# Kernel optimization log

Measured on AMD Instinct MI355X. Metric: run time of the kernel, lower is better.

The kernel has to match this reference:

```python
import jax, jax.numpy as jnp
import numpy as np

B, Q, K, DQ, DK, H, DV = 4, 1024, 1024, 256, 256, 64, 256

def setup_inputs() -> dict:
    key = jax.random.key(0)
    k1, k2, k3, k4, k5, k6 = jax.random.split(key, 6)
    queries = jax.random.normal(k1, (B, Q, DQ), dtype=jnp.float32)
    keys = jax.random.normal(k2, (B, K, DK), dtype=jnp.float32)
    values = jax.random.normal(k3, (B, K, DV), dtype=jnp.float32)
    # learned params (stored as (in, out) so x @ W matches nn.Linear)
    W_q = jax.random.normal(k4, (DQ, H), dtype=jnp.float32) / np.sqrt(DQ)
    W_k = jax.random.normal(k5, (DK, H), dtype=jnp.float32) / np.sqrt(DK)
    w_v = jax.random.normal(k6, (H,), dtype=jnp.float32) / np.sqrt(H)
    return {"queries": queries, "keys": keys, "values": values,
            "W_q": W_q, "W_k": W_k, "w_v": w_v}

def reference(queries, keys, values, W_q, W_k, w_v):
    # projections: [B,Q,H], [B,K,H]
    q = jnp.einsum('bqd,dh->bqh', queries, W_q)
    k = jnp.einsum('bkd,dh->bkh', keys, W_k)
    # broadcast add -> tanh -> reduce with w_v: scores [B,Q,K]
    features = jnp.tanh(q[:, :, None, :] + k[:, None, :, :])  # [B,Q,K,H]
    scores = jnp.einsum('bqkh,h->bqk', features, w_v)
    attn = jax.nn.softmax(scores, axis=-1)  # dropout is identity in eval
    return jnp.einsum('bqk,bkv->bqv', attn, values)
```

## Files before the change

### kernel.cpp

```cpp
#include <hip/hip_runtime.h>

#define Bn 4
#define Qn 1024
#define Kn 1024
#define Dd 256
#define Hh 64
#define Dv 256
#define TQ 16

typedef __attribute__((ext_vector_type(8))) short short8;
typedef __attribute__((ext_vector_type(4))) float floatx4;
typedef __attribute__((ext_vector_type(2))) float floatx2;

__device__ __forceinline__ floatx2 fma2(floatx2 a, floatx2 b, floatx2 c) {
    return __builtin_elementwise_fma(a, b, c);
}
__device__ __forceinline__ floatx2 mk2(float x, float y) {
    floatx2 r; r.x = x; r.y = y; return r;
}

__device__ __forceinline__ short f32_to_bf16(float x) {
    unsigned u = __float_as_uint(x);
    unsigned r = u + 0x7fffu + ((u >> 16) & 1u);
    return (short)(r >> 16);
}
__device__ __forceinline__ float bf16_to_f32(short h) {
    return __uint_as_float(((unsigned)(unsigned short)h) << 16);
}

__global__ __launch_bounds__(256) void prep_kernel(const float* __restrict__ Xq,
                                                   const float* __restrict__ Wq,
                                                   const float* __restrict__ Xk,
                                                   const float* __restrict__ Wk,
                                                   const float* __restrict__ V,
                                                   float* __restrict__ Eq,
                                                   float* __restrict__ Ekt,
                                                   short* __restrict__ Vhi,
                                                   short* __restrict__ Vlo) {
    __shared__ float tile[32 * 261];
    int t = threadIdx.x;
    if (blockIdx.x < 256) {
        int gw = blockIdx.x * 4 + (t >> 6);
        int h = t & 63;
        int side = gw >> 9;
        int row0 = (gw & 511) * 8;
        const float* X = side ? Xk : Xq;
        const float* W = side ? Wk : Wq;
        float acc[8] = {0.f, 0.f, 0.f, 0.f, 0.f, 0.f, 0.f, 0.f};
        for (int d4 = 0; d4 < Dd / 4; ++d4) {
            float w0 = W[(d4 * 4 + 0) * Hh + h];
            float w1 = W[(d4 * 4 + 1) * Hh + h];
            float w2 = W[(d4 * 4 + 2) * Hh + h];
            float w3 = W[(d4 * 4 + 3) * Hh + h];
            #pragma unroll
            for (int r = 0; r < 8; ++r) {
                float4 xv = ((const float4*)(X + (size_t)(row0 + r) * Dd))[d4];
                acc[r] = fmaf(xv.x, w0, acc[r]);
                acc[r] = fmaf(xv.y, w1, acc[r]);
                acc[r] = fmaf(xv.z, w2, acc[r]);
                acc[r] = fmaf(xv.w, w3, acc[r]);
            }
        }
        #pragma unroll
        for (int r = 0; r < 8; ++r) {
            int row = row0 + r;
            float e = __expf(2.f * acc[r]);
            if (!side) {
                Eq[(size_t)row * Hh + h] = e;
            } else {
                int b = row >> 10, k = row & 1023;
                Ekt[((size_t)b * Hh + h) * Kn + k] = e;
            }
        }
    } else {
        int blk = blockIdx.x - 256;
        int b = blk >> 5;
        int kt = blk & 31;
        const float* Vg = V + (b * Kn + kt * 32) * Dv;
        for (int i = 0; i < 8; ++i) {
            int k = i * 4 + (t >> 6);
            int n4 = (t & 63) * 4;
            float4 v = *(const float4*)(Vg + k * Dv + n4);
            tile[k * 261 + n4 + 0] = v.x;
            tile[k * 261 + n4 + 1] = v.y;
            tile[k * 261 + n4 + 2] = v.z;
            tile[k * 261 + n4 + 3] = v.w;
        }
        __syncthreads();
        int wave = t >> 6, l = t & 63;
        int n_in = l & 15, kc = l >> 4;
        for (int p = 0; p < 4; ++p) {
            int nt = wave * 4 + p;
            int n = nt * 16 + n_in;
            short8 hi, lo;
            #pragma unroll
            for (int j = 0; j < 8; ++j) {
                float x = tile[(kc * 8 + j) * 261 + n];
                short hs = f32_to_bf16(x);
                hi[j] = hs;
                lo[j] = f32_to_bf16(x - bf16_to_f32(hs));
            }
            size_t base = (((size_t)(b * 32 + kt) * 16 + nt) * 512) + (size_t)l * 8;
            *(short8*)(Vhi + base) = hi;
            *(short8*)(Vlo + base) = lo;
        }
    }
}

__global__ __launch_bounds__(1024, 4) void attn_kernel(const float* __restrict__ Eq,
                                                       const float* __restrict__ Ekt,
                                                       const short* __restrict__ Vhi,
                                                       const short* __restrict__ Vlo,
                                                       const float* __restrict__ wv,
                                                       float* __restrict__ out) {
    __shared__ __align__(16) unsigned sc[TQ * 1028];
    __shared__ float wsum[16 * TQ];
    __shared__ float rinv_s[TQ];

    int tid = threadIdx.x;
    int blk = blockIdx.x;
    int b = (blk & 7) >> 1;
    int tile = (blk >> 3) * 2 + (blk & 1);
    int qbase = tile * TQ;

    const float* kb = Ekt + (size_t)b * Hh * Kn;
    const float* qp = Eq + (size_t)(b * Qn + qbase) * Hh;
    const float4* wv4 = (const float4*)wv;
    floatx2 s2[TQ / 2];
    #pragma unroll
    for (int i = 0; i < TQ / 2; ++i) { s2[i].x = 0.f; s2[i].y = 0.f; }

    float e0 = kb[0 * Kn + tid];
    float e1 = kb[1 * Kn + tid];
    float e2 = kb[2 * Kn + tid];
    float e3 = kb[3 * Kn + tid];
    floatx2 one2 = mk2(1.f, 1.f);
    for (int h4 = 0; h4 < Hh / 4; ++h4) {
        float n0, n1, n2, n3;
        if (h4 < Hh / 4 - 1) {
            const float* kn = kb + (h4 + 1) * 4 * Kn;
            n0 = kn[0 * Kn + tid];
            n1 = kn[1 * Kn + tid];
            n2 = kn[2 * Kn + tid];
            n3 = kn[3 * Kn + tid];
        }
        float4 w4 = wv4[h4];
        floatx2 e0s = mk2(e0, e0), e1s = mk2(e1, e1);
        floatx2 e2s = mk2(e2, e2), e3s = mk2(e3, e3);
        floatx2 wx = mk2(w4.x, w4.x), wy = mk2(w4.y, w4.y);
        floatx2 wz = mk2(w4.z, w4.z), ww = mk2(w4.w, w4.w);
        #pragma unroll
        for (int qq = 0; qq < TQ; qq += 2) {
            float4 qva = *(const float4*)(qp + qq * Hh + h4 * 4);
            float4 qvb = *(const float4*)(qp + (qq + 1) * Hh + h4 * 4);
            floatx2 A = fma2(mk2(qva.x, qvb.x), e0s, one2);
            floatx2 B = fma2(mk2(qva.y, qvb.y), e1s, one2);
            floatx2 C = fma2(mk2(qva.z, qvb.z), e2s, one2);
            floatx2 D = fma2(mk2(qva.w, qvb.w), e3s, one2);
            floatx2 AB = A * B;
            floatx2 CD = C * D;
            floatx2 ABCD = AB * CD;
            floatx2 NAB = fma2(wx, B, wy * A);
            floatx2 NCD = fma2(wz, D, ww * C);
            floatx2 NUM = fma2(NCD, AB, NAB * CD);
            floatx2 R = mk2(__builtin_amdgcn_rcpf(ABCD.x),
                            __builtin_amdgcn_rcpf(ABCD.y));
            s2[qq >> 1] = fma2(NUM, R, s2[qq >> 1]);
        }
        e0 = n0; e1 = n1; e2 = n2; e3 = n3;
    }

    unsigned short* sp = (unsigned short*)sc;
    float part[TQ];
    #pragma unroll
    for (int q = 0; q < TQ; ++q) {
        float sq = (q & 1) ? s2[q >> 1].y : s2[q >> 1].x;
        float p = __expf(-2.f * sq);
        part[q] = p;
        short hs = f32_to_bf16(p);
        sp[q * 2056 + tid] = (unsigned short)hs;
        sp[q * 2056 + 1024 + tid] = (unsigned short)f32_to_bf16(p - bf16_to_f32(hs));
    }

    int wave = tid >> 6, lane = tid & 63;
    #pragma unroll
    for (int q = 0; q < TQ; ++q) {
        #pragma unroll
        for (int off = 32; off >= 1; off >>= 1)
            part[q] += __shfl_xor(part[q], off, 64);
    }
    if (lane == 0) {
        #pragma unroll
        for (int q = 0; q < TQ; ++q) wsum[wave * TQ + q] = part[q];
    }
    __syncthreads();

    {
        float v = (lane < 16) ? wsum[lane * TQ + wave] : 0.f;
        v += __shfl_xor(v, 8, 64);
        v += __shfl_xor(v, 4, 64);
        v += __shfl_xor(v, 2, 64);
        v += __shfl_xor(v, 1, 64);
        if (lane == 0) rinv_s[wave] = 1.f / v;
    }
    __syncthreads();

    int qf = lane & 15, kc = lane >> 4;
    floatx4 acc = {0.f, 0.f, 0.f, 0.f};
    const char* scb = (const char*)sc;
    for (int kt = 0; kt < 32; ++kt) {
        short8 bhi = *(const short8*)(scb + qf * 4112 + kt * 64 + kc * 16);
        short8 blo = *(const short8*)(scb + qf * 4112 + 2048 + kt * 64 + kc * 16);
        size_t base = (((size_t)(b * 32 + kt) * 16 + wave) * 512) + (size_t)lane * 8;
        short8 ah = *(const short8*)(Vhi + base);
        short8 al = *(const short8*)(Vlo + base);
        acc = __builtin_amdgcn_mfma_f32_16x16x32_bf16(ah, bhi, acc, 0, 0, 0);
        acc = __builtin_amdgcn_mfma_f32_16x16x32_bf16(al, bhi, acc, 0, 0, 0);
        acc = __builtin_amdgcn_mfma_f32_16x16x32_bf16(ah, blo, acc, 0, 0, 0);
    }
    {
        float r = rinv_s[qf];
        float* ob = out + ((size_t)(b * Qn + qbase + qf)) * Dv + wave * 16 + kc * 4;
        float4 o = { acc[0] * r, acc[1] * r, acc[2] * r, acc[3] * r };
        *(float4*)ob = o;
    }
}

extern "C" void kernel_launch(void* const* d_in, const int* in_sizes, int n_in,
                              void* d_out, int out_size, void* d_ws, size_t ws_size,
                              hipStream_t stream) {
    const float* queries = (const float*)d_in[0];
    const float* keys    = (const float*)d_in[1];
    const float* values  = (const float*)d_in[2];
    const float* W_q     = (const float*)d_in[3];
    const float* W_k     = (const float*)d_in[4];
    const float* w_v     = (const float*)d_in[5];
    float* out = (float*)d_out;

    float* Eq  = (float*)d_ws;
    float* Ekt = Eq + Bn * Qn * Hh;
    short* Vhi = (short*)(Ekt + Bn * Kn * Hh);
    short* Vlo = Vhi + (size_t)Bn * Kn * Dv;

    prep_kernel<<<384, 256, 0, stream>>>(queries, W_q, keys, W_k, values,
                                         Eq, Ekt, Vhi, Vlo);
    attn_kernel<<<Bn * (Qn / TQ), 1024, 0, stream>>>(Eq, Ekt, Vhi, Vlo, w_v, out);
}
```

Measured before the change: 124.4 us.

## Split key dimension across two blocks with separate normalization kernel

Each attention block now handles half of the keys (512 threads instead of 1024), writing unnormalized partial outputs and partial softmax sums to workspace. A new norm kernel adds the two halves and divides by the combined sum. The aim is smaller blocks and twice as many of them for better occupancy and load balance. The cost is an extra kernel launch and extra global traffic for the partial results. Softmax has no max subtraction, so adding the partials is exact.

```diff
diff --git a/kernel.cpp b/kernel.cpp
--- a/kernel.cpp
+++ b/kernel.cpp
@@ -107,21 +107,23 @@
     }
 }
 
-__global__ __launch_bounds__(1024, 4) void attn_kernel(const float* __restrict__ Eq,
-                                                       const float* __restrict__ Ekt,
-                                                       const short* __restrict__ Vhi,
-                                                       const short* __restrict__ Vlo,
-                                                       const float* __restrict__ wv,
-                                                       float* __restrict__ out) {
-    __shared__ __align__(16) unsigned sc[TQ * 1028];
-    __shared__ float wsum[16 * TQ];
-    __shared__ float rinv_s[TQ];
+__global__ __launch_bounds__(512, 4) void attn_kernel(const float* __restrict__ Eq,
+                                                      const float* __restrict__ Ekt,
+                                                      const short* __restrict__ Vhi,
+                                                      const short* __restrict__ Vlo,
+                                                      const float* __restrict__ wv,
+                                                      float* __restrict__ Ows,
+                                                      float* __restrict__ Sws) {
+    __shared__ __align__(16) unsigned sc[TQ * 514];
+    __shared__ float wsum[8 * TQ];
 
     int tid = threadIdx.x;
     int blk = blockIdx.x;
     int b = (blk & 7) >> 1;
-    int tile = (blk >> 3) * 2 + (blk & 1);
+    int idx = (blk >> 3) * 2 + (blk & 1);
+    int tile = idx >> 1, half = idx & 1;
     int qbase = tile * TQ;
+    int kglob = half * 512 + tid;
 
     const float* kb = Ekt + (size_t)b * Hh * Kn;
     const float* qp = Eq + (size_t)(b * Qn + qbase) * Hh;
@@ -130,19 +132,19 @@
     #pragma unroll
     for (int i = 0; i < TQ / 2; ++i) { s2[i].x = 0.f; s2[i].y = 0.f; }
 
-    float e0 = kb[0 * Kn + tid];
-    float e1 = kb[1 * Kn + tid];
-    float e2 = kb[2 * Kn + tid];
-    float e3 = kb[3 * Kn + tid];
+    float e0 = kb[0 * Kn + kglob];
+    float e1 = kb[1 * Kn + kglob];
+    float e2 = kb[2 * Kn + kglob];
+    float e3 = kb[3 * Kn + kglob];
     floatx2 one2 = mk2(1.f, 1.f);
     for (int h4 = 0; h4 < Hh / 4; ++h4) {
         float n0, n1, n2, n3;
         if (h4 < Hh / 4 - 1) {
             const float* kn = kb + (h4 + 1) * 4 * Kn;
-            n0 = kn[0 * Kn + tid];
-            n1 = kn[1 * Kn + tid];
-            n2 = kn[2 * Kn + tid];
-            n3 = kn[3 * Kn + tid];
+            n0 = kn[0 * Kn + kglob];
+            n1 = kn[1 * Kn + kglob];
+            n2 = kn[2 * Kn + kglob];
+            n3 = kn[3 * Kn + kglob];
         }
         float4 w4 = wv4[h4];
         floatx2 e0s = mk2(e0, e0), e1s = mk2(e1, e1);
@@ -178,8 +180,8 @@
         float p = __expf(-2.f * sq);
         part[q] = p;
         short hs = f32_to_bf16(p);
-        sp[q * 2056 + tid] = (unsigned short)hs;
-        sp[q * 2056 + 1024 + tid] = (unsigned short)f32_to_bf16(p - bf16_to_f32(hs));
+        sp[q * 1028 + tid] = (unsigned short)hs;
+        sp[q * 1028 + 512 + tid] = (unsigned short)f32_to_bf16(p - bf16_to_f32(hs));
     }
 
     int wave = tid >> 6, lane = tid & 63;
@@ -195,34 +197,59 @@
     }
     __syncthreads();
 
-    {
-        float v = (lane < 16) ? wsum[lane * TQ + wave] : 0.f;
-        v += __shfl_xor(v, 8, 64);
+    #pragma unroll
+    for (int rr = 0; rr < 2; ++rr) {
+        int q = wave + rr * 8;
+        float v = (lane < 8) ? wsum[lane * TQ + q] : 0.f;
         v += __shfl_xor(v, 4, 64);
         v += __shfl_xor(v, 2, 64);
         v += __shfl_xor(v, 1, 64);
-        if (lane == 0) rinv_s[wave] = 1.f / v;
-    }
-    __syncthreads();
+        if (lane == 0)
+            Sws[(size_t)half * (Bn * Qn) + (size_t)(b * Qn + qbase + q)] = v;
+    }
 
     int qf = lane & 15, kc = lane >> 4;
-    floatx4 acc = {0.f, 0.f, 0.f, 0.f};
+    floatx4 acc0 = {0.f, 0.f, 0.f, 0.f};
+    floatx4 acc1 = {0.f, 0.f, 0.f, 0.f};
     const char* scb = (const char*)sc;
-    for (int kt = 0; kt < 32; ++kt) {
-        short8 bhi = *(const short8*)(scb + qf * 4112 + kt * 64 + kc * 16);
-        short8 blo = *(const short8*)(scb + qf * 4112 + 2048 + kt * 64 + kc * 16);
-        size_t base = (((size_t)(b * 32 + kt) * 16 + wave) * 512) + (size_t)lane * 8;
-        short8 ah = *(const short8*)(Vhi + base);
-        short8 al = *(const short8*)(Vlo + base);
-        acc = __builtin_amdgcn_mfma_f32_16x16x32_bf16(ah, bhi, acc, 0, 0, 0);
-        acc = __builtin_amdgcn_mfma_f32_16x16x32_bf16(al, bhi, acc, 0, 0, 0);
-        acc = __builtin_amdgcn_mfma_f32_16x16x32_bf16(ah, blo, acc, 0, 0, 0);
+    for (int kt = 0; kt < 16; ++kt) {
+        short8 bhi = *(const short8*)(scb + qf * 2056 + kt * 64 + kc * 16);
+        short8 blo = *(const short8*)(scb + qf * 2056 + 1024 + kt * 64 + kc * 16);
+        int ktg = half * 16 + kt;
+        size_t base0 = (((size_t)(b * 32 + ktg) * 16 + wave * 2 + 0) * 512) + (size_t)lane * 8;
+        size_t base1 = (((size_t)(b * 32 + ktg) * 16 + wave * 2 + 1) * 512) + (size_t)lane * 8;
+        short8 a0h = *(const short8*)(Vhi + base0);
+        short8 a0l = *(const short8*)(Vlo + base0);
+        short8 a1h = *(const short8*)(Vhi + base1);
+        short8 a1l = *(const short8*)(Vlo + base1);
+        acc0 = __builtin_amdgcn_mfma_f32_16x16x32_bf16(a0h, bhi, acc0, 0, 0, 0);
+        acc0 = __builtin_amdgcn_mfma_f32_16x16x32_bf16(a0l, bhi, acc0, 0, 0, 0);
+        acc0 = __builtin_amdgcn_mfma_f32_16x16x32_bf16(a0h, blo, acc0, 0, 0, 0);
+        acc1 = __builtin_amdgcn_mfma_f32_16x16x32_bf16(a1h, bhi, acc1, 0, 0, 0);
+        acc1 = __builtin_amdgcn_mfma_f32_16x16x32_bf16(a1l, bhi, acc1, 0, 0, 0);
+        acc1 = __builtin_amdgcn_mfma_f32_16x16x32_bf16(a1h, blo, acc1, 0, 0, 0);
     }
     {
-        float r = rinv_s[qf];
-        float* ob = out + ((size_t)(b * Qn + qbase + qf)) * Dv + wave * 16 + kc * 4;
-        float4 o = { acc[0] * r, acc[1] * r, acc[2] * r, acc[3] * r };
-        *(float4*)ob = o;
+        float* ob = Ows + (size_t)half * (Bn * Qn * Dv)
+                  + ((size_t)(b * Qn + qbase + qf)) * Dv + wave * 32 + kc * 4;
+        float4 o0 = { acc0[0], acc0[1], acc0[2], acc0[3] };
+        float4 o1 = { acc1[0], acc1[1], acc1[2], acc1[3] };
+        *(float4*)(ob + 0)  = o0;
+        *(float4*)(ob + 16) = o1;
+    }
+}
+
+__global__ __launch_bounds__(256) void norm_kernel(const float* __restrict__ Ows,
+                                                   const float* __restrict__ Sws,
+                                                   float* __restrict__ out) {
+    int v = threadIdx.x;
+    int r0 = blockIdx.x * 8;
+    #pragma unroll
+    for (int i = 0; i < 8; ++i) {
+        size_t gq = r0 + i;
+        float s = Sws[gq] + Sws[(size_t)(Bn * Qn) + gq];
+        float o = Ows[gq * Dv + v] + Ows[(size_t)(Bn * Qn * Dv) + gq * Dv + v];
+        out[gq * Dv + v] = o * (1.f / s);
     }
 }
 
@@ -241,8 +268,11 @@
     float* Ekt = Eq + Bn * Qn * Hh;
     short* Vhi = (short*)(Ekt + Bn * Kn * Hh);
     short* Vlo = Vhi + (size_t)Bn * Kn * Dv;
+    float* Ows = (float*)(Vlo + (size_t)Bn * Kn * Dv);
+    float* Sws = Ows + (size_t)2 * Bn * Qn * Dv;
 
     prep_kernel<<<384, 256, 0, stream>>>(queries, W_q, keys, W_k, values,
                                          Eq, Ekt, Vhi, Vlo);
-    attn_kernel<<<Bn * (Qn / TQ), 1024, 0, stream>>>(Eq, Ekt, Vhi, Vlo, w_v, out);
-}
+    attn_kernel<<<512, 512, 0, stream>>>(Eq, Ekt, Vhi, Vlo, w_v, Ows, Sws);
+    norm_kernel<<<Bn * Qn / 8, 256, 0, stream>>>(Ows, Sws, out);
+}
```

New measurement: 132.3 us. 1.06x slower.
